# Kernel tuning notes

Measured on AMD Instinct MI355X. Metric: run time of the kernel, lower is better.

Reference implementation:

```python
import math
import jax, jax.numpy as jnp
import numpy as np

B, T, C = 256, 200, 512
H = 8
N_ATTN = 512
HEAD = N_ATTN // H          # 64
ROT = HEAD // 2             # 32 (rotary_ndims = head_size * 0.5)
MAXLEN = 200
ITEM_NUM = 100000


def setup_inputs() -> dict:
    key = jax.random.key(0)
    ks = jax.random.split(key, 16)
    s = 0.02
    item_emb = jax.random.normal(ks[0], (ITEM_NUM + 1, C), jnp.float32) * s
    item_emb = item_emb.at[0].set(0.0)  # padding_idx=0
    inp = {
        "user_ids": jax.random.randint(ks[1], (B,), 0, 10000),
        "log_seqs": jax.random.randint(ks[2], (B, T), 0, ITEM_NUM + 1),
        "pos_seqs": jax.random.randint(ks[3], (B, T), 0, ITEM_NUM + 1),
        "neg_seqs": jax.random.randint(ks[4], (B, T), 0, ITEM_NUM + 1),
        "item_emb": item_emb,
        "time_w": 1.0 + jax.random.normal(ks[5], (H, MAXLEN), jnp.float32) * 0.1,
        "time_alpha": 1.0 + jax.random.normal(ks[6], (H, 1, MAXLEN), jnp.float32) * 0.1,
        "time_beta": 1.0 + jax.random.normal(ks[7], (H, MAXLEN, 1), jnp.float32) * 0.1,
        "time_gamma": 1.0 + jax.random.normal(ks[8], (MAXLEN, 1), jnp.float32) * 0.1,
        "Wq": jax.random.normal(ks[9], (N_ATTN, C), jnp.float32) * s,
        "bq": jnp.zeros((N_ATTN,), jnp.float32),
        "Wk": jax.random.normal(ks[10], (N_ATTN, C), jnp.float32) * s,
        "bk": jnp.zeros((N_ATTN,), jnp.float32),
        "Wv": jax.random.normal(ks[11], (N_ATTN, C), jnp.float32) * s,
        "bv": jnp.zeros((N_ATTN,), jnp.float32),
        "Wmix": jax.random.normal(ks[12], (H, H), jnp.float32) * (1.0 / math.sqrt(H)),
        "Wo": jax.random.normal(ks[13], (C, N_ATTN), jnp.float32) * s,
        "bo": jnp.zeros((C,), jnp.float32),
    }
    return inp


def _rotate_half(x):
    x1, x2 = x[..., : x.shape[-1] // 2], x[..., x.shape[-1] // 2 :]
    return jnp.concatenate((-x2, x1), axis=-1)


def _mha_pro(x_items, time_w, time_alpha, time_beta, time_gamma,
             Wq, bq, Wk, bk, Wv, bv, Wmix, Wo, bo):
    # x_items: [B, T, C]
    TT = MAXLEN
    # Toeplitz time-decay matrix built exactly like the torch pad/tile/reshape trick
    w = jnp.pad(time_w, ((0, 0), (0, TT)))          # [H, 2TT]
    w = jnp.tile(w, (1, TT))                         # [H, 2TT*TT]
    w = w[:, :-TT].reshape(H, TT, 2 * TT - 1)        # [H, TT, 2TT-1]
    w = w[:, :, TT - 1 :]                            # [H, TT, TT]
    w = w[:, :T, :T] * time_alpha[:, :, :T] * time_beta[:, :T, :]  # [H, T, T]

    # time_shift: shift first half of channels down by one token
    half = C // 2
    shifted = jnp.pad(x_items[:, :, :half], ((0, 0), (1, 0), (0, 0)))[:, :-1]
    x = jnp.concatenate([shifted, x_items[:, :, half:]], axis=-1)  # [B, T, C]

    q = (x @ Wq.T + bq).reshape(B, T, H, HEAD).transpose(0, 2, 1, 3)  # [B,H,T,D]
    k = (x @ Wk.T + bk).reshape(B, T, H, HEAD).transpose(0, 2, 1, 3)
    v = (x @ Wv.T + bv).reshape(B, T, H, HEAD).transpose(0, 2, 1, 3)

    # partial rotary on first ROT dims
    q_rot, q_pass = q[..., :ROT], q[..., ROT:]
    k_rot, k_pass = k[..., :ROT], k[..., ROT:]
    inv_freq = 1.0 / (10000.0 ** (jnp.arange(0, ROT, 2, dtype=jnp.float32) / ROT))
    freqs = jnp.arange(T, dtype=jnp.float32)[:, None] * inv_freq[None, :]  # [T, ROT/2]
    emb = jnp.concatenate((freqs, freqs), axis=-1)   # [T, ROT]
    cos, sin = jnp.cos(emb), jnp.sin(emb)
    q_rot = q_rot * cos + _rotate_half(q_rot) * sin
    k_rot = k_rot * cos + _rotate_half(k_rot) * sin
    q = jnp.concatenate((q_rot, q_pass), axis=-1)
    k = jnp.concatenate((k_rot, k_pass), axis=-1)

    att = jnp.einsum('bhtd,bhsd->bhts', q, k) * (1.0 / math.sqrt(HEAD))
    causal = jnp.tril(jnp.ones((T, T), bool))
    att = jnp.where(causal, att, -jnp.inf)
    att = jax.nn.softmax(att, axis=-1)
    att = att * w                                   # learned time-decay mask
    att = jnp.einsum('hg,bgts->bhts', Wmix, att)    # 1x1 conv across heads

    out = jnp.einsum('bhts,bhsd->bhtd', att, v)
    out = out.transpose(0, 2, 1, 3).reshape(B, T, N_ATTN)
    out = (out @ Wo.T + bo) * time_gamma[:T, :]
    return out


def reference(user_ids, log_seqs, pos_seqs, neg_seqs, item_emb,
              time_w, time_alpha, time_beta, time_gamma,
              Wq, bq, Wk, bk, Wv, bv, Wmix, Wo, bo):
    x_items = item_emb[log_seqs]                    # [B, T, C]
    log_feats = _mha_pro(x_items, time_w, time_alpha, time_beta, time_gamma,
                         Wq, bq, Wk, bk, Wv, bv, Wmix, Wo, bo)
    pos_embs = item_emb[pos_seqs]
    neg_embs = item_emb[neg_seqs]
    pos_logits = log_feats * pos_embs               # [B, T, C] (as in source)
    neg_logits = (log_feats * neg_embs).sum(axis=-1)  # [B, T]
    return pos_logits, neg_logits
```

## Files before the change

kernel.cpp:

```cpp
#include <hip/hip_runtime.h>

#define B_    256
#define T_    200
#define C_    512
#define H_    8
#define HEAD_ 64
#define M_    (B_ * T_)
#define POS_OUT_ (M_ * C_)
#define QK_ROWS_ 208
#define VT_PAD_  224
#define P_PAD_   200

typedef __attribute__((ext_vector_type(8))) _Float16 f16x8;
typedef __attribute__((ext_vector_type(4))) _Float16 f16x4;
typedef __attribute__((ext_vector_type(2))) _Float16 f16x2;
typedef __attribute__((ext_vector_type(4))) float f32x4;

__device__ __forceinline__ void gload16(const void* g, void* l) {
    __builtin_amdgcn_global_load_lds(
        (const __attribute__((address_space(1))) unsigned int*)g,
        (__attribute__((address_space(3))) unsigned int*)l, 16, 0, 0);
}

__global__ __launch_bounds__(256) void gather_shift_k(
    const float* __restrict__ emb, const int* __restrict__ logs,
    _Float16* __restrict__ x)
{
    const int total = M_ * 128;
    for (int gid = blockIdx.x * 256 + threadIdx.x; gid < total; gid += gridDim.x * 256) {
        int bt = gid >> 7;
        int c  = (gid & 127) * 4;
        int t  = bt % T_;
        _Float16* xr = x + (size_t)bt * C_ + c;
        if (c < 256) {
            if (t == 0) {
                *(f16x4*)xr = (f16x4){(_Float16)0.f, (_Float16)0.f, (_Float16)0.f, (_Float16)0.f};
                continue;
            }
            float4 v = *(const float4*)(emb + (size_t)logs[bt - 1] * C_ + c);
            *(f16x4*)xr = (f16x4){(_Float16)v.x, (_Float16)v.y, (_Float16)v.z, (_Float16)v.w};
        } else {
            float4 v = *(const float4*)(emb + (size_t)logs[bt] * C_ + c);
            *(f16x4*)xr = (f16x4){(_Float16)v.x, (_Float16)v.y, (_Float16)v.z, (_Float16)v.w};
        }
    }
}

__global__ __launch_bounds__(256) void convert_w_k(
    const float* __restrict__ Wq, const float* __restrict__ Wk,
    const float* __restrict__ Wv, const float* __restrict__ Wo,
    _Float16* __restrict__ dst)
{
    int idx = blockIdx.x * 256 + threadIdx.x;
    int mat = idx >> 16;
    int off = (idx & 65535) << 2;
    const float* src = (mat == 0) ? Wq : (mat == 1) ? Wk : (mat == 2) ? Wv : Wo;
    float4 v = *(const float4*)(src + off);
    f16x4 o = { (_Float16)v.x, (_Float16)v.y, (_Float16)v.z, (_Float16)v.w };
    *(f16x4*)(dst + ((size_t)mat << 18) + off) = o;
}

__global__ __launch_bounds__(256) void wtab_k(
    const float* __restrict__ tw, const float* __restrict__ ta,
    const float* __restrict__ tb, float* __restrict__ wtab)
{
    int idx = blockIdx.x * 256 + threadIdx.x;
    int g   = idx / (208 * 208);
    int rem = idx % (208 * 208);
    int t = rem / 208, s = rem % 208;
    int tt = min(t, 199), ss = min(s, 199);
    int wi = min(max(199 - tt + ss, 0), 199);
    wtab[idx] = tw[g * 200 + wi] * ta[g * 200 + ss] * tb[g * 200 + tt];
}

__global__ __launch_bounds__(256) void zero_neg_k(float* __restrict__ out)
{
    out[(size_t)POS_OUT_ + blockIdx.x * 256 + threadIdx.x] = 0.0f;
}

__global__ __launch_bounds__(256) void zero_pads_k(
    _Float16* __restrict__ Qb, _Float16* __restrict__ Kb,
    _Float16* __restrict__ Vt)
{
    int bh = blockIdx.x;
    int tid = threadIdx.x;
    for (int idx = tid; idx < 8 * 64; idx += 256) {
        Qb[(size_t)bh * QK_ROWS_ * 64 + 200 * 64 + idx] = (_Float16)0.0f;
        Kb[(size_t)bh * QK_ROWS_ * 64 + 200 * 64 + idx] = (_Float16)0.0f;
    }
    for (int idx = tid; idx < 64 * (VT_PAD_ - 200); idx += 256) {
        int d = idx / (VT_PAD_ - 200), s = 200 + idx % (VT_PAD_ - 200);
        Vt[(size_t)bh * 64 * VT_PAD_ + (size_t)d * VT_PAD_ + s] = (_Float16)0.0f;
    }
}

__global__ __launch_bounds__(256) void gemm_qkv_k(
    const _Float16* __restrict__ xh,
    const _Float16* __restrict__ Wh,
    const float* __restrict__ bq, const float* __restrict__ bk, const float* __restrict__ bv,
    _Float16* __restrict__ Qb, _Float16* __restrict__ Kb,
    _Float16* __restrict__ Vt,
    int nmt)
{
    int n = blockIdx.x;
    int mt, v;
    if ((nmt & 7) == 0) { int q8 = n & 7, i = n >> 3; mt = (i / 12) * 8 + q8; v = i % 12; }
    else               { mt = n / 12; v = n % 12; }
    int which = v >> 2;
    int nt    = v & 3;
    int m0    = mt * 128;
    const _Float16* Wm = Wh + ((size_t)(which * 4 + nt) * 128) * 512;
    const float* bias = (which == 0) ? bq : (which == 1) ? bk : bv;

    __shared__ _Float16 As[3][128 * 32];
    __shared__ _Float16 Bs[3][128 * 32];

    int tid  = threadIdx.x;
    int w    = tid >> 6, lane = tid & 63;
    int quad = lane >> 4, l15 = lane & 15;
    int wm   = w >> 1,    wn  = w & 1;
    int srow = lane >> 2, scg = lane & 3;
    int scg_src = scg ^ ((srow >> 1) & 3);
    int rq = (l15 >> 1) & 3;

    auto stage = [&](int buf, int k0) {
#pragma unroll
        for (int rr = 0; rr < 2; ++rr) {
            int seg = rr * 4 + w;
            int row = seg * 16 + srow;
            gload16(xh + (size_t)(m0 + row) * 512 + k0 + scg_src * 8, As[buf] + seg * 512);
            gload16(Wm + (size_t)row * 512 + k0 + scg_src * 8, Bs[buf] + seg * 512);
        }
    };

    f32x4 acc[4][4];
#pragma unroll
    for (int m = 0; m < 4; ++m)
#pragma unroll
        for (int nn = 0; nn < 4; ++nn) acc[m][nn] = (f32x4){0.f, 0.f, 0.f, 0.f};

    stage(0, 0);
    stage(1, 32);
#pragma unroll
    for (int s = 0; s < 16; ++s) {
        if (s < 15) asm volatile("s_waitcnt vmcnt(4)" ::: "memory");
        else        asm volatile("s_waitcnt vmcnt(0)" ::: "memory");
        __builtin_amdgcn_s_barrier();
        __builtin_amdgcn_sched_barrier(0);
        const _Float16* Ab = As[s % 3];
        const _Float16* Bb = Bs[s % 3];
        f16x8 af[4], bf[4];
#pragma unroll
        for (int m = 0; m < 4; ++m)
            af[m] = *(const f16x8*)(Ab + (wm * 4 + m) * 512 + l15 * 32 + (quad ^ rq) * 8);
#pragma unroll
        for (int nn = 0; nn < 4; ++nn)
            bf[nn] = *(const f16x8*)(Bb + (wn * 4 + nn) * 512 + l15 * 32 + (quad ^ rq) * 8);
        if (s <= 13) stage((s + 2) % 3, (s + 2) * 32);
#pragma unroll
        for (int m = 0; m < 4; ++m)
#pragma unroll
            for (int nn = 0; nn < 4; ++nn)
                acc[m][nn] = __builtin_amdgcn_mfma_f32_16x16x32_f16(af[m], bf[nn], acc[m][nn], 0, 0, 0);
    }

    int h = nt * 2 + wn;
    if (which < 2) {
        _Float16* dst = (which == 0) ? Qb : Kb;
        float sc = (which == 0) ? 0.125f : 1.0f;
        float invf = powf(10000.0f, -(float)l15 / 16.0f);
#pragma unroll
        for (int m = 0; m < 4; ++m) {
#pragma unroll
            for (int r = 0; r < 4; ++r) {
                int row = m0 + wm * 64 + m * 16 + quad * 4 + r;
                int bl = row / T_, t = row % T_;
                float sn, cs;
                __sincosf((float)t * invf, &sn, &cs);
                size_t base = ((size_t)(bl * 8 + h) * QK_ROWS_ + t) * 64;
                float av = acc[m][0][r] + bias[h * 64 + l15];
                float bv2 = acc[m][1][r] + bias[h * 64 + 16 + l15];
                dst[base + l15]      = (_Float16)((av * cs - bv2 * sn) * sc);
                dst[base + 16 + l15] = (_Float16)((bv2 * cs + av * sn) * sc);
                dst[base + 32 + l15] = (_Float16)((acc[m][2][r] + bias[h * 64 + 32 + l15]) * sc);
                dst[base + 48 + l15] = (_Float16)((acc[m][3][r] + bias[h * 64 + 48 + l15]) * sc);
            }
        }
    } else {
#pragma unroll
        for (int nn = 0; nn < 4; ++nn) {
            int ch = nn * 16 + l15;
            float bval = bias[h * 64 + ch];
#pragma unroll
            for (int m = 0; m < 4; ++m) {
                int r0 = m0 + wm * 64 + m * 16 + quad * 4;
                int t0v = r0 % T_;
                if (t0v <= 196) {
                    int bl = r0 / T_;
                    f16x4 v4 = {(_Float16)(acc[m][nn][0] + bval),
                                (_Float16)(acc[m][nn][1] + bval),
                                (_Float16)(acc[m][nn][2] + bval),
                                (_Float16)(acc[m][nn][3] + bval)};
                    *(f16x4*)(Vt + ((size_t)(bl * 8 + h) * 64 + ch) * VT_PAD_ + t0v) = v4;
                } else {
#pragma unroll
                    for (int r = 0; r < 4; ++r) {
                        int rw = r0 + r;
                        int bl = rw / T_, s = rw % T_;
                        Vt[((size_t)(bl * 8 + h) * 64 + ch) * VT_PAD_ + s] = (_Float16)(acc[m][nn][r] + bval);
                    }
                }
            }
        }
    }
}

__global__ __launch_bounds__(512, 4) void attn_fused_k(
    const _Float16* __restrict__ Qb, const _Float16* __restrict__ Kb,
    const _Float16* __restrict__ Vt,
    const float* __restrict__ wtab,
    const float* __restrict__ wmix,
    _Float16* __restrict__ ao)
{
    int n    = blockIdx.x;
    int xcd  = n & 7, slot = n >> 3;
    int i_tile = 12 - (slot % 13);
    int b      = (slot / 13) * 8 + xcd;

    int tid  = threadIdx.x;
    int wave = tid >> 6, lane = tid & 63;
    int quad = lane >> 4, l15 = lane & 15;
    int t0   = i_tile * 16;
    int nst  = i_tile + 1;
    int smax = nst * 16;
    int lim  = smax < 200 ? smax : 200;

    __shared__ _Float16 Pt[8][16][P_PAD_];
    __shared__ float mixs[64];
    __shared__ f16x2 invt[8][16];

    if (tid < 64) mixs[tid] = wmix[tid];

    {
        int g = wave;
        int trow = quad * 4;
        const _Float16* Qg = Qb + (size_t)(b * 8 + g) * QK_ROWS_ * 64;
        const _Float16* Kg = Kb + (size_t)(b * 8 + g) * QK_ROWS_ * 64;
        f16x8 a0 = *(const f16x8*)(Qg + (size_t)(t0 + l15) * 64 + quad * 8);
        f16x8 a1 = *(const f16x8*)(Qg + (size_t)(t0 + l15) * 64 + quad * 8 + 32);
        const float* wg = wtab + ((size_t)g * 208 + t0) * 208;

        f16x8 kr0[3], kr1[3];
        float wr[3][4];
        kr0[0] = *(const f16x8*)(Kg + (size_t)l15 * 64 + quad * 8);
        kr1[0] = *(const f16x8*)(Kg + (size_t)l15 * 64 + quad * 8 + 32);
#pragma unroll
        for (int r = 0; r < 4; ++r) wr[0][r] = wg[(trow + r) * 208 + l15];
        if (nst > 1) {
            kr0[1] = *(const f16x8*)(Kg + (size_t)(16 + l15) * 64 + quad * 8);
            kr1[1] = *(const f16x8*)(Kg + (size_t)(16 + l15) * 64 + quad * 8 + 32);
#pragma unroll
            for (int r = 0; r < 4; ++r) wr[1][r] = wg[(trow + r) * 208 + 16 + l15];
        }
        __builtin_amdgcn_sched_barrier(0);

        float sum[4] = {0.f, 0.f, 0.f, 0.f};
        __builtin_amdgcn_s_setprio(1);
#pragma unroll
        for (int st = 0; st < 13; ++st) if (st < nst) {
            if (st + 2 < nst) {
                int sl = (st + 2) % 3;
                kr0[sl] = *(const f16x8*)(Kg + (size_t)((st + 2) * 16 + l15) * 64 + quad * 8);
                kr1[sl] = *(const f16x8*)(Kg + (size_t)((st + 2) * 16 + l15) * 64 + quad * 8 + 32);
#pragma unroll
                for (int r = 0; r < 4; ++r) wr[sl][r] = wg[(trow + r) * 208 + (st + 2) * 16 + l15];
                __builtin_amdgcn_sched_barrier(0);
            }
            int cl = st % 3;
            f32x4 c = {0.f, 0.f, 0.f, 0.f};
            c = __builtin_amdgcn_mfma_f32_16x16x32_f16(a0, kr0[cl], c, 0, 0, 0);
            c = __builtin_amdgcn_mfma_f32_16x16x32_f16(a1, kr1[cl], c, 0, 0, 0);
            int s = st * 16 + l15;
            bool diag = (st == nst - 1);
#pragma unroll
            for (int r = 0; r < 4; ++r) {
                int t = t0 + trow + r;
                float e = (!diag || s <= t) ? __expf(c[r]) : 0.f;
                sum[r] += e;
                if (s < 200) Pt[g][trow + r][s] = (_Float16)(e * wr[cl][r]);
            }
        }
        __builtin_amdgcn_s_setprio(0);
#pragma unroll
        for (int r = 0; r < 4; ++r) {
            float sm = sum[r];
            sm += __shfl_xor(sm, 1);
            sm += __shfl_xor(sm, 2);
            sm += __shfl_xor(sm, 4);
            sm += __shfl_xor(sm, 8);
            if (l15 == 0) {
                _Float16 ih = (_Float16)(1.0f / sm);
                invt[g][trow + r] = (f16x2){ih, ih};
            }
        }
    }
    __syncthreads();

    {
        f16x2 mx[64];
#pragma unroll
        for (int i = 0; i < 64; ++i) {
            _Float16 mh = (_Float16)mixs[i];
            mx[i] = (f16x2){mh, mh};
        }
        int nitems = lim << 3;
        for (int idx = tid; idx < nitems; idx += 512) {
            int tloc = idx & 15;
            int sp   = (idx >> 4) << 1;
            f16x2 pv[8];
#pragma unroll
            for (int g = 0; g < 8; ++g) pv[g] = *(const f16x2*)&Pt[g][tloc][sp];
#pragma unroll
            for (int g = 0; g < 8; ++g) pv[g] = pv[g] * invt[g][tloc];
#pragma unroll
            for (int ho = 0; ho < 8; ++ho) {
                f16x2 o = mx[ho * 8] * pv[0];
#pragma unroll
                for (int g = 1; g < 8; ++g) o += mx[ho * 8 + g] * pv[g];
                *(f16x2*)&Pt[ho][tloc][sp] = o;
            }
        }
    }
    __syncthreads();

    {
        int nk = (nst + 1) >> 1;
        int hda = wave;
        const _Float16* Vh = Vt + (size_t)(b * 8 + hda) * 64 * VT_PAD_;
        f32x4 c4[4];
#pragma unroll
        for (int n2 = 0; n2 < 4; ++n2) c4[n2] = (f32x4){0.f, 0.f, 0.f, 0.f};
        f16x8 vb[2][4];
#pragma unroll
        for (int n2 = 0; n2 < 4; ++n2)
            vb[0][n2] = *(const f16x8*)(Vh + (size_t)(n2 * 16 + l15) * VT_PAD_ + quad * 8);
        __builtin_amdgcn_s_setprio(1);
#pragma unroll
        for (int ks = 0; ks < 7; ++ks) if (ks < nk) {
            if (ks + 1 < nk) {
#pragma unroll
                for (int n2 = 0; n2 < 4; ++n2)
                    vb[(ks + 1) & 1][n2] = *(const f16x8*)(Vh + (size_t)(n2 * 16 + l15) * VT_PAD_ + (ks + 1) * 32 + quad * 8);
                __builtin_amdgcn_sched_barrier(0);
            }
            int cc = ks * 32 + quad * 8;
            bool oob = cc >= lim;
            int cl = oob ? 0 : cc;
            f16x8 a = *(const f16x8*)(&Pt[hda][l15][cl]);
            if (oob) {
#pragma unroll
                for (int j = 0; j < 8; ++j) a[j] = (_Float16)0.0f;
            }
#pragma unroll
            for (int n2 = 0; n2 < 4; ++n2)
                c4[n2] = __builtin_amdgcn_mfma_f32_16x16x32_f16(a, vb[ks & 1][n2], c4[n2], 0, 0, 0);
        }
        __builtin_amdgcn_s_setprio(0);
#pragma unroll
        for (int n2 = 0; n2 < 4; ++n2)
#pragma unroll
            for (int r = 0; r < 4; ++r) {
                int t = t0 + quad * 4 + r;
                if (t < 200)
                    ao[((size_t)(b * T_ + t)) * 512 + hda * 64 + n2 * 16 + l15] = (_Float16)c4[n2][r];
            }
    }
}

__global__ __launch_bounds__(256) void gemm_out_k(
    const _Float16* __restrict__ Ah, const _Float16* __restrict__ Woh,
    const float* __restrict__ bo, const float* __restrict__ gamma,
    const float* __restrict__ emb, const int* __restrict__ pos,
    const int* __restrict__ neg, float* __restrict__ out,
    int bt0, int nmt)
{
    int n = blockIdx.x;
    int mt, nt;
    if ((nmt & 7) == 0) { int q8 = n & 7, i = n >> 3; mt = (i / 4) * 8 + q8; nt = i % 4; }
    else               { mt = n / 4; nt = n % 4; }
    int m0 = mt * 128;
    const _Float16* Wm = Woh + (size_t)nt * 128 * 512;

    __shared__ _Float16 As[3][128 * 32];
    __shared__ _Float16 Bs[3][128 * 32];

    int tid  = threadIdx.x;
    int w    = tid >> 6, lane = tid & 63;
    int quad = lane >> 4, l15 = lane & 15;
    int wm   = w >> 1,    wn  = w & 1;
    int srow = lane >> 2, scg = lane & 3;
    int scg_src = scg ^ ((srow >> 1) & 3);
    int rq = (l15 >> 1) & 3;

    auto stage = [&](int buf, int k0) {
#pragma unroll
        for (int rr = 0; rr < 2; ++rr) {
            int seg = rr * 4 + w;
            int row = seg * 16 + srow;
            gload16(Ah + (size_t)(m0 + row) * 512 + k0 + scg_src * 8, As[buf] + seg * 512);
            gload16(Wm + (size_t)row * 512 + k0 + scg_src * 8, Bs[buf] + seg * 512);
        }
    };

    f32x4 acc[4][4];
#pragma unroll
    for (int m = 0; m < 4; ++m)
#pragma unroll
        for (int nn = 0; nn < 4; ++nn) acc[m][nn] = (f32x4){0.f, 0.f, 0.f, 0.f};

    stage(0, 0);
    stage(1, 32);
#pragma unroll
    for (int s = 0; s < 16; ++s) {
        if (s < 15) asm volatile("s_waitcnt vmcnt(4)" ::: "memory");
        else        asm volatile("s_waitcnt vmcnt(0)" ::: "memory");
        __builtin_amdgcn_s_barrier();
        __builtin_amdgcn_sched_barrier(0);
        const _Float16* Ab = As[s % 3];
        const _Float16* Bb = Bs[s % 3];
        f16x8 af[4], bf[4];
#pragma unroll
        for (int m = 0; m < 4; ++m)
            af[m] = *(const f16x8*)(Ab + (wm * 4 + m) * 512 + l15 * 32 + (quad ^ rq) * 8);
#pragma unroll
        for (int nn = 0; nn < 4; ++nn)
            bf[nn] = *(const f16x8*)(Bb + (wn * 4 + nn) * 512 + l15 * 32 + (quad ^ rq) * 8);
        if (s <= 13) stage((s + 2) % 3, (s + 2) * 32);
#pragma unroll
        for (int m = 0; m < 4; ++m)
#pragma unroll
            for (int nn = 0; nn < 4; ++nn)
                acc[m][nn] = __builtin_amdgcn_mfma_f32_16x16x32_f16(af[m], bf[nn], acc[m][nn], 0, 0, 0);
    }

#pragma unroll
    for (int m = 0; m < 4; ++m) {
#pragma unroll
        for (int r = 0; r < 4; ++r) {
            int row = m0 + wm * 64 + m * 16 + quad * 4 + r;
            float gg = gamma[row % T_];
            int pr = pos[row], nr = neg[row];
            const float* pe = emb + (size_t)pr * 512;
            const float* ne = emb + (size_t)nr * 512;
            float* po = out + (size_t)(bt0 + row) * 512;
            float s = 0.f;
#pragma unroll
            for (int nn = 0; nn < 4; ++nn) {
                int col = nt * 128 + wn * 64 + nn * 16 + l15;
                float val = (acc[m][nn][r] + bo[col]) * gg;
                po[col] = val * pe[col];
                s += val * ne[col];
            }
            s += __shfl_xor(s, 1);
            s += __shfl_xor(s, 2);
            s += __shfl_xor(s, 4);
            s += __shfl_xor(s, 8);
            if (l15 == 0)
                atomicAdd(out + (size_t)POS_OUT_ + bt0 + row, s);
        }
    }
}

extern "C" void kernel_launch(void* const* d_in, const int* in_sizes, int n_in,
                              void* d_out, int out_size, void* d_ws, size_t ws_size,
                              hipStream_t stream)
{
    const int* logs = (const int*)d_in[1];
    const int* pos  = (const int*)d_in[2];
    const int* neg  = (const int*)d_in[3];
    const float* emb = (const float*)d_in[4];
    const float* tw  = (const float*)d_in[5];
    const float* ta  = (const float*)d_in[6];
    const float* tb  = (const float*)d_in[7];
    const float* tg  = (const float*)d_in[8];
    const float* Wq  = (const float*)d_in[9];
    const float* bq  = (const float*)d_in[10];
    const float* Wk  = (const float*)d_in[11];
    const float* bk  = (const float*)d_in[12];
    const float* Wv  = (const float*)d_in[13];
    const float* bv  = (const float*)d_in[14];
    const float* wmix= (const float*)d_in[15];
    const float* Wo  = (const float*)d_in[16];
    const float* bo  = (const float*)d_in[17];

    const size_t PER_B = (size_t)T_ * C_ * 2
                       + (size_t)8 * QK_ROWS_ * 64 * 2
                       + (size_t)8 * QK_ROWS_ * 64 * 2
                       + (size_t)8 * 64 * VT_PAD_ * 2
                       + (size_t)T_ * C_ * 2;
    const size_t SZ_WH = (size_t)4 * 512 * 512 * 2;
    const size_t SZ_WT = (size_t)8 * 208 * 208 * 4;

    int CB = (ws_size >= SZ_WH + SZ_WT + PER_B * B_) ? B_ : 32;
    int nch = B_ / CB;
    int CM = CB * T_;
    int NMT = CM / 128;

    char* p = (char*)d_ws;
    _Float16*       Wh   = (_Float16*)p;  p += SZ_WH;
    float*          wtab = (float*)p;     p += SZ_WT;
    _Float16*       xh   = (_Float16*)p;  p += (size_t)CM * C_ * 2;
    _Float16*       Qb   = (_Float16*)p;  p += (size_t)CB * 8 * QK_ROWS_ * 64 * 2;
    _Float16*       Kb   = (_Float16*)p;  p += (size_t)CB * 8 * QK_ROWS_ * 64 * 2;
    _Float16*       Vt   = (_Float16*)p;  p += (size_t)CB * 8 * 64 * VT_PAD_ * 2;
    _Float16*       aoh  = (_Float16*)p;

    convert_w_k<<<1024, 256, 0, stream>>>(Wq, Wk, Wv, Wo, Wh);
    wtab_k<<<1352, 256, 0, stream>>>(tw, ta, tb, wtab);
    zero_neg_k<<<M_ / 256, 256, 0, stream>>>((float*)d_out);
    zero_pads_k<<<CB * 8, 256, 0, stream>>>(Qb, Kb, Vt);

    for (int c = 0; c < nch; ++c) {
        int bt0 = c * CM;
        gather_shift_k<<<2048, 256, 0, stream>>>(emb, logs + bt0, xh);
        gemm_qkv_k<<<NMT * 12, 256, 0, stream>>>(xh, Wh, bq, bk, bv, Qb, Kb, Vt, NMT);
        attn_fused_k<<<13 * CB, 512, 0, stream>>>(Qb, Kb, Vt, wtab, wmix, aoh);
        gemm_out_k<<<NMT * 4, 256, 0, stream>>>(aoh, Wh + (size_t)3 * 512 * 512, bo, tg,
                                                emb, pos + bt0, neg + bt0, (float*)d_out, bt0, NMT);
    }
}
```

Measured before the change: 664.4 us.

## Fuse embedding gather and token shift into QKV GEMM A-tile loading

Drops the separate gather_shift kernel and its fp16 staging buffer. The QKV GEMM now reads fp32 embedding rows directly through the log-sequence indices, applying the token shift to the first 256 channels, converts them to fp16 in registers and writes them to swizzled LDS. This avoids a full write and re-read of the x activation through global memory and one kernel launch. In exchange, each A tile is re-gathered by all 12 N-tile blocks, so fp32 embedding traffic is read 12 times and goes through registers instead of direct-to-LDS loads, with adjusted waitcnt pipelining.

```diff
diff --git a/kernel.cpp b/kernel.cpp
--- a/kernel.cpp
+++ b/kernel.cpp
@@ -22,30 +22,6 @@
         (__attribute__((address_space(3))) unsigned int*)l, 16, 0, 0);
 }
 
-__global__ __launch_bounds__(256) void gather_shift_k(
-    const float* __restrict__ emb, const int* __restrict__ logs,
-    _Float16* __restrict__ x)
-{
-    const int total = M_ * 128;
-    for (int gid = blockIdx.x * 256 + threadIdx.x; gid < total; gid += gridDim.x * 256) {
-        int bt = gid >> 7;
-        int c  = (gid & 127) * 4;
-        int t  = bt % T_;
-        _Float16* xr = x + (size_t)bt * C_ + c;
-        if (c < 256) {
-            if (t == 0) {
-                *(f16x4*)xr = (f16x4){(_Float16)0.f, (_Float16)0.f, (_Float16)0.f, (_Float16)0.f};
-                continue;
-            }
-            float4 v = *(const float4*)(emb + (size_t)logs[bt - 1] * C_ + c);
-            *(f16x4*)xr = (f16x4){(_Float16)v.x, (_Float16)v.y, (_Float16)v.z, (_Float16)v.w};
-        } else {
-            float4 v = *(const float4*)(emb + (size_t)logs[bt] * C_ + c);
-            *(f16x4*)xr = (f16x4){(_Float16)v.x, (_Float16)v.y, (_Float16)v.z, (_Float16)v.w};
-        }
-    }
-}
-
 __global__ __launch_bounds__(256) void convert_w_k(
     const float* __restrict__ Wq, const float* __restrict__ Wk,
     const float* __restrict__ Wv, const float* __restrict__ Wo,
@@ -95,7 +71,7 @@
 }
 
 __global__ __launch_bounds__(256) void gemm_qkv_k(
-    const _Float16* __restrict__ xh,
+    const float* __restrict__ emb, const int* __restrict__ logs,
     const _Float16* __restrict__ Wh,
     const float* __restrict__ bq, const float* __restrict__ bk, const float* __restrict__ bv,
     _Float16* __restrict__ Qb, _Float16* __restrict__ Kb,
@@ -123,12 +99,42 @@
     int scg_src = scg ^ ((srow >> 1) & 3);
     int rq = (l15 >> 1) & 3;
 
-    auto stage = [&](int buf, int k0) {
+    int r0l = tid >> 2;
+    int cg  = tid & 3;
+    int asw = ((r0l & 15) >> 1) & 3;
+    int csrc = (cg ^ asw) * 8;
+    int rowg0 = m0 + r0l, rowg1 = m0 + 64 + r0l;
+    int idxC0 = logs[rowg0], idxC1 = logs[rowg1];
+    int idxP0 = (rowg0 % T_) ? logs[rowg0 - 1] : -1;
+    int idxP1 = (rowg1 % T_) ? logs[rowg1 - 1] : -1;
+
+    float4 a0, a1, b0, b1;
+    auto ldA = [&](int k0) {
+        int c = k0 + csrc;
+        int i0 = (k0 < 256) ? idxP0 : idxC0;
+        int i1 = (k0 < 256) ? idxP1 : idxC1;
+        if (i0 >= 0) {
+            a0 = *(const float4*)(emb + (size_t)i0 * 512 + c);
+            a1 = *(const float4*)(emb + (size_t)i0 * 512 + c + 4);
+        } else { a0 = (float4){0,0,0,0}; a1 = (float4){0,0,0,0}; }
+        if (i1 >= 0) {
+            b0 = *(const float4*)(emb + (size_t)i1 * 512 + c);
+            b1 = *(const float4*)(emb + (size_t)i1 * 512 + c + 4);
+        } else { b0 = (float4){0,0,0,0}; b1 = (float4){0,0,0,0}; }
+    };
+    auto wrA = [&](int buf) {
+        f16x8 h0 = {(_Float16)a0.x, (_Float16)a0.y, (_Float16)a0.z, (_Float16)a0.w,
+                    (_Float16)a1.x, (_Float16)a1.y, (_Float16)a1.z, (_Float16)a1.w};
+        *(f16x8*)(As[buf] + r0l * 32 + cg * 8) = h0;
+        f16x8 h1 = {(_Float16)b0.x, (_Float16)b0.y, (_Float16)b0.z, (_Float16)b0.w,
+                    (_Float16)b1.x, (_Float16)b1.y, (_Float16)b1.z, (_Float16)b1.w};
+        *(f16x8*)(As[buf] + (64 + r0l) * 32 + cg * 8) = h1;
+    };
+    auto stageB = [&](int buf, int k0) {
 #pragma unroll
         for (int rr = 0; rr < 2; ++rr) {
             int seg = rr * 4 + w;
             int row = seg * 16 + srow;
-            gload16(xh + (size_t)(m0 + row) * 512 + k0 + scg_src * 8, As[buf] + seg * 512);
             gload16(Wm + (size_t)row * 512 + k0 + scg_src * 8, Bs[buf] + seg * 512);
         }
     };
@@ -139,12 +145,16 @@
 #pragma unroll
         for (int nn = 0; nn < 4; ++nn) acc[m][nn] = (f32x4){0.f, 0.f, 0.f, 0.f};
 
-    stage(0, 0);
-    stage(1, 32);
+    ldA(0);
+    stageB(0, 0);
+    wrA(0);
+    ldA(32);
+    stageB(1, 32);
+
 #pragma unroll
     for (int s = 0; s < 16; ++s) {
-        if (s < 15) asm volatile("s_waitcnt vmcnt(4)" ::: "memory");
-        else        asm volatile("s_waitcnt vmcnt(0)" ::: "memory");
+        if (s < 15) asm volatile("s_waitcnt vmcnt(6) lgkmcnt(0)" ::: "memory");
+        else        asm volatile("s_waitcnt vmcnt(0) lgkmcnt(0)" ::: "memory");
         __builtin_amdgcn_s_barrier();
         __builtin_amdgcn_sched_barrier(0);
         const _Float16* Ab = As[s % 3];
@@ -156,7 +166,8 @@
 #pragma unroll
         for (int nn = 0; nn < 4; ++nn)
             bf[nn] = *(const f16x8*)(Bb + (wn * 4 + nn) * 512 + l15 * 32 + (quad ^ rq) * 8);
-        if (s <= 13) stage((s + 2) % 3, (s + 2) * 32);
+        if (s <= 14) wrA((s + 1) % 3);
+        if (s <= 13) { ldA((s + 2) * 32); stageB((s + 2) % 3, (s + 2) * 32); }
 #pragma unroll
         for (int m = 0; m < 4; ++m)
 #pragma unroll
@@ -493,8 +504,7 @@
     const float* Wo  = (const float*)d_in[16];
     const float* bo  = (const float*)d_in[17];
 
-    const size_t PER_B = (size_t)T_ * C_ * 2
-                       + (size_t)8 * QK_ROWS_ * 64 * 2
+    const size_t PER_B = (size_t)8 * QK_ROWS_ * 64 * 2
                        + (size_t)8 * QK_ROWS_ * 64 * 2
                        + (size_t)8 * 64 * VT_PAD_ * 2
                        + (size_t)T_ * C_ * 2;
@@ -509,7 +519,6 @@
     char* p = (char*)d_ws;
     _Float16*       Wh   = (_Float16*)p;  p += SZ_WH;
     float*          wtab = (float*)p;     p += SZ_WT;
-    _Float16*       xh   = (_Float16*)p;  p += (size_t)CM * C_ * 2;
     _Float16*       Qb   = (_Float16*)p;  p += (size_t)CB * 8 * QK_ROWS_ * 64 * 2;
     _Float16*       Kb   = (_Float16*)p;  p += (size_t)CB * 8 * QK_ROWS_ * 64 * 2;
     _Float16*       Vt   = (_Float16*)p;  p += (size_t)CB * 8 * 64 * VT_PAD_ * 2;
@@ -522,8 +531,7 @@
 
     for (int c = 0; c < nch; ++c) {
         int bt0 = c * CM;
-        gather_shift_k<<<2048, 256, 0, stream>>>(emb, logs + bt0, xh);
-        gemm_qkv_k<<<NMT * 12, 256, 0, stream>>>(xh, Wh, bq, bk, bv, Qb, Kb, Vt, NMT);
+        gemm_qkv_k<<<NMT * 12, 256, 0, stream>>>(emb, logs + bt0, Wh, bq, bk, bv, Qb, Kb, Vt, NMT);
         attn_fused_k<<<13 * CB, 512, 0, stream>>>(Qb, Kb, Vt, wtab, wmix, aoh);
         gemm_out_k<<<NMT * 4, 256, 0, stream>>>(aoh, Wh + (size_t)3 * 512 * 512, bo, tg,
                                                 emb, pos + bt0, neg + bt0, (float*)d_out, bt0, NMT);
```

New measurement: 794.6 us. 1.2x slower.
